# Kernel optimization log

Hardware: AMD Instinct MI355X
Metric: run time of the kernel (lower is better)

Reference implementation:

```python
import jax, jax.numpy as jnp
import numpy as np

N = 50000      # nodes
K = 17         # regular degree (edges per node, pre-sorted by row)
D_IN = 128
D_OUT = 64
E = N * K


def setup_inputs() -> dict:
    key = jax.random.key(0)
    k1, k2, k3, k4, k5 = jax.random.split(key, 5)
    x = jax.random.normal(k1, (N, D_IN), dtype=jnp.float32)
    # edges sorted by row (required by dimmedian_idx); regular degree K
    row = jnp.repeat(jnp.arange(N, dtype=jnp.int32), K)
    col = jax.random.randint(k2, (E,), 0, N, dtype=jnp.int32)
    edge_index = jnp.stack([row, col], axis=0)
    edge_weight = jax.random.uniform(k3, (E,), dtype=jnp.float32)
    # glorot-style linear weight, zero-init-like small bias
    weight = jax.random.normal(k4, (D_IN, D_OUT), dtype=jnp.float32) * np.float32(1.0 / np.sqrt(D_IN))
    bias = jax.random.normal(k5, (D_OUT,), dtype=jnp.float32) * np.float32(0.01)
    return {"x": x, "edge_index": edge_index, "edge_weight": edge_weight,
            "weight": weight, "bias": bias}


def _weighted_dim_median(xp, col, w):
    """Per-node, per-dimension weighted median over neighbors (dimmedian_idx + gather).
    xp: [N, D] projected features; col: [E] neighbor ids; w: [E] edge weights.
    Exploits the regular degree K: edges for node i occupy rows i*K:(i+1)*K.
    """
    D = xp.shape[1]
    vals = xp[col].reshape(N, K, D)            # neighbor features per node
    wN = jnp.broadcast_to(w.reshape(N, K)[:, :, None], (N, K, D))
    order = jnp.argsort(vals, axis=1)          # sort neighbors per dim by value
    sorted_vals = jnp.take_along_axis(vals, order, axis=1)
    sorted_w = jnp.take_along_axis(wN, order, axis=1)
    cum = jnp.cumsum(sorted_w, axis=1)
    total = cum[:, -1:, :]
    # first sorted position where cumulative weight reaches half the total
    med_pos = jnp.argmax(cum >= 0.5 * total, axis=1)      # [N, D]
    med = jnp.take_along_axis(sorted_vals, med_pos[:, None, :], axis=1)[:, 0, :]
    return med


def reference(x, edge_index, edge_weight, weight, bias):
    xp = x @ weight                            # lin projection (no bias)
    row, col = edge_index[0], edge_index[1]
    med = _weighted_dim_median(xp, col, edge_weight)      # soft_median_reduce
    # row normalization: scatter_add of edge weights per destination row
    row_sum = jax.ops.segment_sum(edge_weight, row, num_segments=N)
    return row_sum[:, None] * med + bias
```

## Files before the change

kernel.cpp:

```cpp
#include <hip/hip_runtime.h>

#define N_NODES 50000
#define K_DEG   17
#define DIN     128
#define DOUT    64

typedef _Float16 f16;
typedef __attribute__((ext_vector_type(8))) short  short8;
typedef __attribute__((ext_vector_type(4))) float  floatx4;

struct CEPair { unsigned char a, b; };

constexpr int net_count(int n) {
  int t = 0; while ((1 << t) < n) ++t;
  int cnt = 0;
  for (int p = 1 << (t - 1); p > 0; p >>= 1) {
    int q = 1 << (t - 1), r = 0, d = p;
    for (;;) {
      for (int i = 0; i < n - d; ++i)
        if ((i & p) == r) ++cnt;
      if (q == p) break;
      d = q - p; q >>= 1; r = p;
    }
  }
  return cnt;
}

template <int NP> struct NetArr { CEPair v[NP]; };

template <int NP>
constexpr NetArr<NP> net_pairs(int n) {
  NetArr<NP> out{};
  int t = 0; while ((1 << t) < n) ++t;
  int cnt = 0;
  for (int p = 1 << (t - 1); p > 0; p >>= 1) {
    int q = 1 << (t - 1), r = 0, d = p;
    for (;;) {
      for (int i = 0; i < n - d; ++i)
        if ((i & p) == r) {
          out.v[cnt].a = (unsigned char)i;
          out.v[cnt].b = (unsigned char)(i + d);
          ++cnt;
        }
      if (q == p) break;
      d = q - p; q >>= 1; r = p;
    }
  }
  return out;
}

constexpr int NP17 = net_count(K_DEG);

__device__ __forceinline__ unsigned int f2bf(float f) {
  union { float f; unsigned int u; } c; c.f = f;
  return (c.u + 0x7FFFu + ((c.u >> 16) & 1u)) >> 16;
}
__device__ __forceinline__ float bf2f(unsigned int b) {
  union { float f; unsigned int u; } c; c.u = b << 16;
  return c.f;
}

__global__ void convw_kernel(const float* __restrict__ W,
                             unsigned short* __restrict__ T) {
  const int flat = blockIdx.x * 256 + threadIdx.x;
  const int j    = flat & 7;
  const int lane = (flat >> 3) & 63;
  const int pair = flat >> 9;
  const int ks   = pair >> 2, nt = pair & 3;
  const int k    = ks * 32 + (lane >> 4) * 8 + j;
  const int n    = nt * 16 + (lane & 15);
  const float f  = W[k * DOUT + n];
  const unsigned int hb = f2bf(f);
  const float        lo = f - bf2f(hb);
  const unsigned int lb = f2bf(lo);
  T[flat]        = (unsigned short)hb;
  T[flat + 8192] = (unsigned short)lb;
}

__global__ __launch_bounds__(256) void gemm_kernel(
    const float* __restrict__ x, const unsigned short* __restrict__ T,
    f16* __restrict__ xp) {
  const int gwave = blockIdx.x * 4 + (threadIdx.x >> 6);
  if (gwave >= (N_NODES / 16)) return;
  const int lane = threadIdx.x & 63;
  const int r0 = gwave * 16;
  const int m  = lane & 15;
  const int q  = lane >> 4;

  const float4* x4 = (const float4*)x;
  float4 xr[8];
  #pragma unroll
  for (int ks = 0; ks < 4; ++ks) {
    const int base = (r0 + m) * (DIN / 4) + ks * 8 + q * 2;
    xr[ks * 2 + 0] = x4[base + 0];
    xr[ks * 2 + 1] = x4[base + 1];
  }

  floatx4 acc[4];
  #pragma unroll
  for (int nt = 0; nt < 4; ++nt) acc[nt] = (floatx4){0.f, 0.f, 0.f, 0.f};

  const short8* Th = (const short8*)T;
  const short8* Tl = (const short8*)(T + 8192);

  #pragma unroll
  for (int ks = 0; ks < 4; ++ks) {
    short8 Bh[4], Bl[4];
    #pragma unroll
    for (int nt = 0; nt < 4; ++nt) {
      const int fi = (ks * 4 + nt) * 64 + lane;
      Bh[nt] = Th[fi];
      Bl[nt] = Tl[fi];
    }
    float f[8] = {xr[ks*2].x, xr[ks*2].y, xr[ks*2].z, xr[ks*2].w,
                  xr[ks*2+1].x, xr[ks*2+1].y, xr[ks*2+1].z, xr[ks*2+1].w};
    union { unsigned int i[4]; short8 s; } Ah, Al;
    #pragma unroll
    for (int r = 0; r < 4; ++r) {
      const unsigned int h0 = f2bf(f[2*r]),   h1 = f2bf(f[2*r+1]);
      const unsigned int l0 = f2bf(f[2*r]   - bf2f(h0));
      const unsigned int l1 = f2bf(f[2*r+1] - bf2f(h1));
      Ah.i[r] = h0 | (h1 << 16);
      Al.i[r] = l0 | (l1 << 16);
    }
    #pragma unroll
    for (int nt = 0; nt < 4; ++nt) {
      acc[nt] = __builtin_amdgcn_mfma_f32_16x16x32_bf16(Al.s, Bh[nt], acc[nt], 0, 0, 0);
      acc[nt] = __builtin_amdgcn_mfma_f32_16x16x32_bf16(Ah.s, Bl[nt], acc[nt], 0, 0, 0);
      acc[nt] = __builtin_amdgcn_mfma_f32_16x16x32_bf16(Ah.s, Bh[nt], acc[nt], 0, 0, 0);
    }
  }

  #pragma unroll
  for (int nt = 0; nt < 4; ++nt) {
    const int col = nt * 16 + m;
    #pragma unroll
    for (int r = 0; r < 4; ++r)
      xp[(r0 + q * 4 + r) * DOUT + col] = (f16)acc[nt][r];
  }
}

__global__ __launch_bounds__(512) void median_kernel(
    const f16* __restrict__ xp, const int* __restrict__ col,
    const float* __restrict__ ew, const float* __restrict__ bias,
    float* __restrict__ out) {
  __shared__ float wlds[8 * 32];

  const int wave = threadIdx.x >> 6;
  const int lane = threadIdx.x & 63;
  const int node = __builtin_amdgcn_readfirstlane(blockIdx.x * 8 + wave);

  const int*   cp = col + node * K_DEG;
  const float* wp = ew  + node * K_DEG;

  int c[K_DEG];
  #pragma unroll
  for (int j = 0; j < K_DEG; ++j) c[j] = cp[j];

  float v[K_DEG];
  v[16] = (float)xp[c[16] * DOUT + lane];
  #pragma unroll
  for (int j = 0; j < K_DEG - 1; ++j)
    v[j] = (float)xp[c[j] * DOUT + lane];

  float* wl = wlds + wave * 32;
  if (lane < K_DEG) wl[lane] = wp[lane];

  const float bl = bias[lane];

  #pragma unroll
  for (int j = 0; j < K_DEG; ++j) {
    union { float f; unsigned int u; } c2; c2.f = v[j];
    c2.u |= (unsigned)(j * 4);
    v[j] = c2.f;
  }

  constexpr NetArr<NP17> NET = net_pairs<NP17>(K_DEG);
  #pragma unroll
  for (int s = 0; s < NP17; ++s) {
    const int a = NET.v[s].a, b = NET.v[s].b;
    const float va = v[a], vb = v[b];
    v[a] = fminf(va, vb);
    v[b] = fmaxf(va, vb);
  }

  const unsigned base = (unsigned)(wave * 128);
  const char* wbytes = (const char*)wlds;
  float run = 0.f, cum[K_DEG];
  #pragma unroll
  for (int j = 0; j < K_DEG; ++j) {
    union { float f; unsigned int u; } c2; c2.f = v[j];
    const float swj = *(const float*)(wbytes + ((c2.u & 0x7Cu) | base));
    run += swj; cum[j] = run;
  }
  const float half = 0.5f * run;

  float med = v[K_DEG - 1];
  #pragma unroll
  for (int j = K_DEG - 2; j >= 0; --j)
    med = (cum[j] >= half) ? v[j] : med;

  out[node * DOUT + lane] = run * med + bl;
}

extern "C" void kernel_launch(void* const* d_in, const int* in_sizes, int n_in,
                              void* d_out, int out_size, void* d_ws, size_t ws_size,
                              hipStream_t stream) {
  const float* x    = (const float*)d_in[0];
  const int*   ei   = (const int*)d_in[1];
  const float* ew   = (const float*)d_in[2];
  const float* W    = (const float*)d_in[3];
  const float* bias = (const float*)d_in[4];
  float*       out  = (float*)d_out;

  f16*            xp = (f16*)d_ws;
  unsigned short* T  = (unsigned short*)((char*)d_ws + (size_t)N_NODES * DOUT * 2);
  const int*      colp = ei + (size_t)N_NODES * K_DEG;

  convw_kernel<<<8192 / 256, 256, 0, stream>>>(W, T);
  gemm_kernel<<<(N_NODES / 16 + 3) / 4, 256, 0, stream>>>(x, T, xp);
  median_kernel<<<N_NODES / 8, 512, 0, stream>>>(xp, colp, ew, bias, out);
}
```

Before: 119.2 us.

## Split projected features into two 32-column planes for cache-local gathers

The GEMM now writes the fp16 projection as two planes of 32 columns each instead of one row-major array of 64 columns. The median kernel runs twice, once per plane, and each wave handles two nodes with 32 dimensions per half-wave. Each plane is half the size, so the random neighbor gathers have a smaller working set that fits better in L2/MALL. The cost is a second launch, loading the edge indices and weights twice, and 64-byte gather segments per neighbor instead of 128-byte ones.

```diff
diff --git a/kernel.cpp b/kernel.cpp
--- a/kernel.cpp
+++ b/kernel.cpp
@@ -79,7 +79,7 @@
 
 __global__ __launch_bounds__(256) void gemm_kernel(
     const float* __restrict__ x, const unsigned short* __restrict__ T,
-    f16* __restrict__ xp) {
+    f16* __restrict__ pA, f16* __restrict__ pB) {
   const int gwave = blockIdx.x * 4 + (threadIdx.x >> 6);
   if (gwave >= (N_NODES / 16)) return;
   const int lane = threadIdx.x & 63;
@@ -134,39 +134,49 @@
   #pragma unroll
   for (int nt = 0; nt < 4; ++nt) {
     const int col = nt * 16 + m;
+    f16* plane = (nt < 2) ? pA : pB;
+    const int d = col & 31;
     #pragma unroll
     for (int r = 0; r < 4; ++r)
-      xp[(r0 + q * 4 + r) * DOUT + col] = (f16)acc[nt][r];
+      plane[(r0 + q * 4 + r) * 32 + d] = (f16)acc[nt][r];
   }
 }
 
 __global__ __launch_bounds__(512) void median_kernel(
-    const f16* __restrict__ xp, const int* __restrict__ col,
+    const f16* __restrict__ plane, const int* __restrict__ col,
     const float* __restrict__ ew, const float* __restrict__ bias,
-    float* __restrict__ out) {
-  __shared__ float wlds[8 * 32];
+    float* __restrict__ out, int dbase) {
+  __shared__ float wlds[8 * 64];
 
   const int wave = threadIdx.x >> 6;
   const int lane = threadIdx.x & 63;
-  const int node = __builtin_amdgcn_readfirstlane(blockIdx.x * 8 + wave);
-
-  const int*   cp = col + node * K_DEG;
-  const float* wp = ew  + node * K_DEG;
-
-  int c[K_DEG];
-  #pragma unroll
-  for (int j = 0; j < K_DEG; ++j) c[j] = cp[j];
+  const int half = lane >> 5;
+  const int d    = lane & 31;
+  const int n0 = __builtin_amdgcn_readfirstlane((blockIdx.x * 8 + wave) * 2);
+
+  const int*   cp = col + n0 * K_DEG;
+  const float* wp = ew  + n0 * K_DEG;
+
+  int c0[K_DEG], c1[K_DEG];
+  #pragma unroll
+  for (int j = 0; j < K_DEG; ++j) { c0[j] = cp[j]; c1[j] = cp[K_DEG + j]; }
 
   float v[K_DEG];
-  v[16] = (float)xp[c[16] * DOUT + lane];
-  #pragma unroll
-  for (int j = 0; j < K_DEG - 1; ++j)
-    v[j] = (float)xp[c[j] * DOUT + lane];
-
-  float* wl = wlds + wave * 32;
-  if (lane < K_DEG) wl[lane] = wp[lane];
-
-  const float bl = bias[lane];
+  #pragma unroll
+  for (int j = 0; j < K_DEG; ++j) {
+    const int cc = half ? c1[j] : c0[j];
+    v[j] = (float)plane[cc * 32 + d];
+  }
+
+  {
+    float* wb = wlds + wave * 64;
+    if (lane < 2 * K_DEG) {
+      const float wv = wp[lane];
+      wb[(lane < K_DEG) ? lane : (32 + lane - K_DEG)] = wv;
+    }
+  }
+
+  const float bl = bias[dbase + d];
 
   #pragma unroll
   for (int j = 0; j < K_DEG; ++j) {
@@ -184,7 +194,7 @@
     v[b] = fmaxf(va, vb);
   }
 
-  const unsigned base = (unsigned)(wave * 128);
+  const unsigned base = (unsigned)(wave * 256 + half * 128);
   const char* wbytes = (const char*)wlds;
   float run = 0.f, cum[K_DEG];
   #pragma unroll
@@ -193,14 +203,14 @@
     const float swj = *(const float*)(wbytes + ((c2.u & 0x7Cu) | base));
     run += swj; cum[j] = run;
   }
-  const float half = 0.5f * run;
+  const float half_t = 0.5f * run;
 
   float med = v[K_DEG - 1];
   #pragma unroll
   for (int j = K_DEG - 2; j >= 0; --j)
-    med = (cum[j] >= half) ? v[j] : med;
-
-  out[node * DOUT + lane] = run * med + bl;
+    med = (cum[j] >= half_t) ? v[j] : med;
+
+  out[(n0 + half) * DOUT + dbase + d] = run * med + bl;
 }
 
 extern "C" void kernel_launch(void* const* d_in, const int* in_sizes, int n_in,
@@ -213,11 +223,13 @@
   const float* bias = (const float*)d_in[4];
   float*       out  = (float*)d_out;
 
-  f16*            xp = (f16*)d_ws;
-  unsigned short* T  = (unsigned short*)((char*)d_ws + (size_t)N_NODES * DOUT * 2);
-  const int*      colp = ei + (size_t)N_NODES * K_DEG;
+  f16* pA = (f16*)d_ws;
+  f16* pB = pA + (size_t)N_NODES * 32;
+  unsigned short* T = (unsigned short*)(pB + (size_t)N_NODES * 32);
+  const int* colp = ei + (size_t)N_NODES * K_DEG;
 
   convw_kernel<<<8192 / 256, 256, 0, stream>>>(W, T);
-  gemm_kernel<<<(N_NODES / 16 + 3) / 4, 256, 0, stream>>>(x, T, xp);
-  median_kernel<<<N_NODES / 8, 512, 0, stream>>>(xp, colp, ew, bias, out);
-}
+  gemm_kernel<<<(N_NODES / 16 + 3) / 4, 256, 0, stream>>>(x, T, pA, pB);
+  median_kernel<<<N_NODES / 16, 512, 0, stream>>>(pA, colp, ew, bias, out, 0);
+  median_kernel<<<N_NODES / 16, 512, 0, stream>>>(pB, colp, ew, bias, out, 32);
+}
```

Measured after the change: 128.1 us. 1.07x slower.
